# Optimization experiments

Hardware: AMD Instinct MI355X
Metric: run time of the kernel (lower is better)

The kernel has to match this reference:

```python
import jax, jax.numpy as jnp
import numpy as np

K = 3
STRIDE = 1
PAD = K // 2
GN_GROUPS = 32
EPS = 1e-5


def _conv(x, w, b, stride, pad):
    y = jax.lax.conv_general_dilated(
        x, w, window_strides=(stride, stride),
        padding=[(pad, pad), (pad, pad)],
        dimension_numbers=("NCHW", "OIHW", "NCHW"))
    return y + b[None, :, None, None]


def _bilinear_gather(img, ys, xs):
    # img: [B,C,H,W]; ys/xs: [B,P,Ho,Wo] float sampling coords (zero padding outside)
    B, C, H, W = img.shape
    y0 = jnp.floor(ys)
    x0 = jnp.floor(xs)
    y1, x1 = y0 + 1.0, x0 + 1.0
    wy1 = ys - y0  # weight toward y1
    wx1 = xs - x0
    wy0 = 1.0 - wy1
    wx0 = 1.0 - wx1
    img_flat = img.reshape(B, C, H * W)

    def corner(yc, xc, wgt):
        yi = yc.astype(jnp.int32)
        xi = xc.astype(jnp.int32)
        valid = (yi >= 0) & (yi < H) & (xi >= 0) & (xi < W)
        idx = jnp.clip(yi, 0, H - 1) * W + jnp.clip(xi, 0, W - 1)  # [B,P,Ho,Wo]
        Bp, P, Ho, Wo = idx.shape
        idx_f = jnp.broadcast_to(idx.reshape(B, 1, P * Ho * Wo), (B, C, P * Ho * Wo))
        vals = jnp.take_along_axis(img_flat, idx_f, axis=2).reshape(B, C, P, Ho, Wo)
        w_eff = jnp.where(valid, wgt, 0.0)[:, None]  # [B,1,P,Ho,Wo]
        return vals * w_eff

    out = (corner(y0, x0, wy0 * wx0) + corner(y0, x1, wy0 * wx1)
           + corner(y1, x0, wy1 * wx0) + corner(y1, x1, wy1 * wx1))
    return out  # [B,C,P,Ho,Wo]


def _deform_conv_gn_relu(x, w_off, b_off, w, b, gamma, beta):
    B, C_in, H, W = x.shape
    C_out = w.shape[0]
    P = K * K
    # offset-predicting conv: [B, 2*P, Ho, Wo], channel order (dy0,dx0,dy1,dx1,...)
    off = _conv(x, w_off, b_off, STRIDE, PAD)
    Ho, Wo = off.shape[2], off.shape[3]
    off = off.reshape(B, P, 2, Ho, Wo)
    dy, dx = off[:, :, 0], off[:, :, 1]  # [B,P,Ho,Wo]
    ky, kx = jnp.meshgrid(jnp.arange(K, dtype=x.dtype), jnp.arange(K, dtype=x.dtype), indexing="ij")
    ky, kx = ky.reshape(P), kx.reshape(P)
    base_y = (jnp.arange(Ho, dtype=x.dtype) * STRIDE - PAD)
    base_x = (jnp.arange(Wo, dtype=x.dtype) * STRIDE - PAD)
    ys = base_y[None, None, :, None] + ky[None, :, None, None] + dy
    xs = base_x[None, None, None, :] + kx[None, :, None, None] + dx
    cols = _bilinear_gather(x, ys, xs)  # [B,C_in,P,Ho,Wo]
    y = jnp.einsum("bcphw,ocp->bohw", cols, w.reshape(C_out, C_in, P)) + b[None, :, None, None]
    # GroupNorm(32, C_out)
    G = GN_GROUPS
    yg = y.reshape(B, G, (C_out // G) * Ho * Wo)
    mu = yg.mean(axis=2, keepdims=True)
    var = yg.var(axis=2, keepdims=True)
    yn = ((yg - mu) * jax.lax.rsqrt(var + EPS)).reshape(B, C_out, Ho, Wo)
    yn = yn * gamma[None, :, None, None] + beta[None, :, None, None]
    return jax.nn.relu(yn)


def setup_inputs() -> dict:
    key = jax.random.key(0)
    ks = jax.random.split(key, 7)
    B, C_in, C_out, H, W = 4, 256, 256, 64, 64
    P = K * K
    fan = C_in * P
    x = jax.random.normal(ks[0], (B, C_in, H, W), dtype=jnp.float32)
    w_off = jax.random.normal(ks[1], (2 * P, C_in, K, K), dtype=jnp.float32) * 0.01
    b_off = jnp.zeros((2 * P,), dtype=jnp.float32)
    w = jax.random.normal(ks[2], (C_out, C_in, K, K), dtype=jnp.float32) / np.sqrt(fan)
    b = jax.random.normal(ks[3], (C_out,), dtype=jnp.float32) * 0.01
    gamma = jnp.ones((C_out,), dtype=jnp.float32)
    beta = jnp.zeros((C_out,), dtype=jnp.float32)
    return {"x": x, "w_off": w_off, "b_off": b_off, "w": w, "b": b, "gamma": gamma, "beta": beta}


def reference(x, w_off, b_off, w, b, gamma, beta):
    return _deform_conv_gn_relu(x, w_off, b_off, w, b, gamma, beta)
```

## Files before the change

### kernel.cpp

```cpp
#include <hip/hip_runtime.h>
#include <hip/hip_bf16.h>

using bf16 = __hip_bfloat16;
typedef __attribute__((ext_vector_type(4))) float f32x4;
typedef __attribute__((ext_vector_type(2))) float f32x2;
typedef __attribute__((ext_vector_type(8))) __bf16 bf16x8;
typedef __attribute__((ext_vector_type(4))) __bf16 bf16x4;

#define CIN 256
#define COUT 256
#define HW 4096
#define NB 4
#define NTOT 16384
#define KDIM 2304

__global__ __launch_bounds__(256) void k_pre(const float* __restrict__ x,
                                             const float* __restrict__ w,
                                             const float* __restrict__ wof,
                                             bf16* __restrict__ xt,
                                             bf16* __restrict__ A,
                                             float* __restrict__ wt) {
  int bid = blockIdx.x;
  int tid = threadIdx.x;
  if (bid < 2048) {
    __shared__ float t[64][33];
    int ct = bid & 3;
    int hwt = (bid >> 2) & 127;
    int b = bid >> 9;
    int c0 = ct * 64, hw0 = hwt * 32;
    const float* xb = x + (size_t)b * CIN * HW;
    int cc = tid >> 5, ww = tid & 31;
#pragma unroll
    for (int pass = 0; pass < 8; ++pass)
      t[cc + pass * 8][ww] = xb[(size_t)(c0 + cc + pass * 8) * HW + hw0 + ww];
    __syncthreads();
    int hwl = tid >> 3, ce = (tid & 7) * 8;
    bf16x8 v;
#pragma unroll
    for (int e = 0; e < 8; ++e) v[e] = (__bf16)t[ce + e][hwl];
    *(bf16x8*)(xt + ((size_t)b * HW + hw0 + hwl) * CIN + c0 + ce) = v;
  } else if (bid < 4352) {
    int i = (bid - 2048) * 256 + tid;
    int o = i / KDIM, r = i % KDIM;
    int p = r >> 8, c = r & 255;
    A[i] = __float2bfloat16(w[((size_t)o * 256 + c) * 9 + p]);
  } else {
    int i = (bid - 4352) * 256 + tid;
    if (i < 18 * CIN * 9) {
      int oc = i % 18;
      int cp = i / 18;
      int c = cp / 9, p = cp % 9;
      wt[i] = wof[((size_t)oc * CIN + c) * 9 + p];
    }
  }
}

__global__ __launch_bounds__(256) void k_convoff2(const float* __restrict__ x,
                                                  const float* __restrict__ wt,
                                                  float* __restrict__ part) {
  __shared__ float lds[8][6][68];
  int bid = blockIdx.x;
  int chunk = bid & 7;
  int rt = (bid >> 3) & 15;
  int b = bid >> 7;
  int tid = threadIdx.x;
  int wq = tid & 63, r = tid >> 6;
  int h0 = rt * 4;
  int c0 = chunk * 32;

  if (tid < 96) {
    int cl = tid / 12, rem = tid % 12;
    lds[cl][rem >> 1][(rem & 1) ? 66 : 1] = 0.f;
  }

  float acc[18];
#pragma unroll
  for (int o = 0; o < 18; ++o) acc[o] = 0.f;

  int ch = tid >> 5, l32 = tid & 31;
  const float* xb = x + (size_t)b * CIN * HW;

  for (int cs = 0; cs < 32; cs += 8) {
    __syncthreads();
    const float* xp = xb + (size_t)(c0 + cs + ch) * HW;
#pragma unroll
    for (int r6 = 0; r6 < 6; ++r6) {
      int hh = h0 - 1 + r6;
      f32x2 v = {0.f, 0.f};
      if ((unsigned)hh < 64u) v = *(const f32x2*)(xp + hh * 64 + l32 * 2);
      *(f32x2*)&lds[ch][r6][2 + l32 * 2] = v;
    }
    __syncthreads();
#pragma unroll
    for (int cl = 0; cl < 8; ++cl) {
      int c = c0 + cs + cl;
      const float* wc = wt + (size_t)c * 9 * 18;
      float xv[9];
#pragma unroll
      for (int ky = 0; ky < 3; ++ky)
#pragma unroll
        for (int kx = 0; kx < 3; ++kx)
          xv[ky * 3 + kx] = lds[cl][r + ky][1 + wq + kx];
#pragma unroll
      for (int p = 0; p < 9; ++p)
#pragma unroll
        for (int o = 0; o < 18; ++o)
          acc[o] = fmaf(xv[p], wc[p * 18 + o], acc[o]);
    }
  }

  float* pp = part + (size_t)chunk * (NB * 18 * HW) + (size_t)b * 18 * HW +
              (h0 + r) * 64 + wq;
#pragma unroll
  for (int o = 0; o < 18; ++o) pp[(size_t)o * HW] = acc[o];
}

__global__ __launch_bounds__(256) void k_offreduce(const float* __restrict__ part,
                                                   const float* __restrict__ boff,
                                                   float* __restrict__ off) {
  int i = blockIdx.x * 256 + threadIdx.x;
  int e0 = i * 4;
  int oc = (e0 >> 12) % 18;
  float bo = boff[oc];
  f32x4 s = {bo, bo, bo, bo};
#pragma unroll
  for (int c = 0; c < 8; ++c) s += *(const f32x4*)(part + (size_t)c * (NB * 18 * HW) + e0);
  *(f32x4*)(off + e0) = s;
}

__global__ __launch_bounds__(256) void k_gather(const bf16* __restrict__ xt,
                                                const float* __restrict__ off,
                                                bf16* __restrict__ colsT) {
  int tid = threadIdx.x;
  int wv = tid >> 6, l = tid & 63;
  int n = blockIdx.x * 4 + wv;
  int hw = n & 4095;
  int b = n >> 12;
  int h = hw >> 6, wq = hw & 63;
  const bf16* xtb = xt + (size_t)b * HW * CIN + l * 4;
  const float* offb = off + (size_t)b * 18 * HW + hw;
  bf16* outp = colsT + (size_t)n * KDIM + l * 4;
#pragma unroll
  for (int p = 0; p < 9; ++p) {
    float dy = offb[(size_t)(2 * p) * HW];
    float dx = offb[(size_t)(2 * p + 1) * HW];
    float ysf = (float)(h - 1 + p / 3) + dy;
    float xsf = (float)(wq - 1 + p % 3) + dx;
    float y0f = floorf(ysf), x0f = floorf(xsf);
    float wy1 = ysf - y0f, wx1 = xsf - x0f;
    float wy0 = 1.f - wy1, wx0 = 1.f - wx1;
    int y0 = (int)y0f, x0 = (int)x0f;
    int y1 = y0 + 1, x1 = x0 + 1;
    float w00 = wy0 * wx0, w01 = wy0 * wx1, w10 = wy1 * wx0, w11 = wy1 * wx1;
    bool vy0 = (unsigned)y0 < 64u, vy1 = (unsigned)y1 < 64u;
    bool vx0 = (unsigned)x0 < 64u, vx1 = (unsigned)x1 < 64u;
    w00 = (vy0 && vx0) ? w00 : 0.f;
    w01 = (vy0 && vx1) ? w01 : 0.f;
    w10 = (vy1 && vx0) ? w10 : 0.f;
    w11 = (vy1 && vx1) ? w11 : 0.f;
    int y0c = min(max(y0, 0), 63), y1c = min(max(y1, 0), 63);
    int x0c = min(max(x0, 0), 63), x1c = min(max(x1, 0), 63);
    bf16x4 c00 = *(const bf16x4*)(xtb + (size_t)(y0c * 64 + x0c) * CIN);
    bf16x4 c01 = *(const bf16x4*)(xtb + (size_t)(y0c * 64 + x1c) * CIN);
    bf16x4 c10 = *(const bf16x4*)(xtb + (size_t)(y1c * 64 + x0c) * CIN);
    bf16x4 c11 = *(const bf16x4*)(xtb + (size_t)(y1c * 64 + x1c) * CIN);
    bf16x4 o;
#pragma unroll
    for (int k = 0; k < 4; ++k) {
      float v = w00 * (float)c00[k] + w01 * (float)c01[k] +
                w10 * (float)c10[k] + w11 * (float)c11[k];
      o[k] = (__bf16)v;
    }
    *(bf16x4*)(outp + p * 256) = o;
  }
}

__global__ __launch_bounds__(512) void k_gemm(const bf16* __restrict__ A,
                                              const bf16* __restrict__ Bt,
                                              const float* __restrict__ bias,
                                              bf16* __restrict__ Y0,
                                              bf16* __restrict__ Y1) {
  __shared__ bf16 As[2][256 * 64];
  __shared__ bf16 Bs[2][64 * 64];
  int bid = blockIdx.x;
  int swz = (bid & 7) * 64 + (bid >> 3);
  int n0 = (swz >> 1) * 64;
  int khalf = swz & 1;
  int tid = threadIdx.x;
  int lane = tid & 63;
  int wave = tid >> 6;
  int wr = (wave >> 1) * 64;
  int wc = (wave & 1) * 32;
  f32x4 acc[4][2];
#pragma unroll
  for (int i = 0; i < 4; ++i)
#pragma unroll
    for (int j = 0; j < 2; ++j) acc[i][j] = (f32x4){0.f, 0.f, 0.f, 0.f};

  int srow = tid >> 3;
  int skdst = (tid & 7) * 8;
  int sksrc = ((tid & 7) ^ ((tid >> 3) & 7)) * 8;
  int kbase = khalf * 18;
  auto stage = [&](int buf, int kt) {
    int k0 = (kbase + kt) * 64;
#pragma unroll
    for (int ps = 0; ps < 4; ++ps) {
      int r = srow + ps * 64;
      __builtin_amdgcn_global_load_lds(
          (const __attribute__((address_space(1))) void*)(A + (size_t)r * KDIM + k0 + sksrc),
          (__attribute__((address_space(3))) void*)(&As[buf][r * 64 + skdst]), 16, 0, 0);
    }
    __builtin_amdgcn_global_load_lds(
        (const __attribute__((address_space(1))) void*)(Bt + (size_t)(n0 + srow) * KDIM + k0 + sksrc),
        (__attribute__((address_space(3))) void*)(&Bs[buf][srow * 64 + skdst]), 16, 0, 0);
  };

  stage(0, 0);
  int rl = lane & 15;
  int kb = (lane >> 4) * 8;
  int xorv = (rl & 7) * 8;
  for (int kt = 0; kt < 18; ++kt) {
    __syncthreads();
    if (kt + 1 < 18) stage((kt + 1) & 1, kt + 1);
    const bf16* as = As[kt & 1];
    const bf16* bs = Bs[kt & 1];
#pragma unroll
    for (int kh = 0; kh < 2; ++kh) {
      int kc = (kh * 32 + kb) ^ xorv;
      bf16x8 af[4], bfr[2];
#pragma unroll
      for (int i = 0; i < 4; ++i)
        af[i] = *(const bf16x8*)(as + (wr + i * 16 + rl) * 64 + kc);
#pragma unroll
      for (int j = 0; j < 2; ++j)
        bfr[j] = *(const bf16x8*)(bs + (wc + j * 16 + rl) * 64 + kc);
#pragma unroll
      for (int i = 0; i < 4; ++i)
#pragma unroll
        for (int j = 0; j < 2; ++j)
          acc[i][j] = __builtin_amdgcn_mfma_f32_16x16x32_bf16(af[i], bfr[j], acc[i][j], 0, 0, 0);
    }
  }

  int cl = lane & 15, rg = (lane >> 4) * 4;
  bf16* Yp = khalf ? Y1 : Y0;
#pragma unroll
  for (int i = 0; i < 4; ++i) {
    int ob = wr + i * 16 + rg;
#pragma unroll
    for (int j = 0; j < 2; ++j) {
      int nn = n0 + wc + j * 16 + cl;
#pragma unroll
      for (int r = 0; r < 4; ++r) {
        float yv = acc[i][j][r] + (khalf ? 0.f : bias[ob + r]);
        Yp[(size_t)(ob + r) * NTOT + nn] = __float2bfloat16(yv);
      }
    }
  }
}

__global__ __launch_bounds__(1024) void k_gnapply(const bf16* __restrict__ Y0,
                                                  const bf16* __restrict__ Y1,
                                                  const float* __restrict__ gamma,
                                                  const float* __restrict__ beta,
                                                  float* __restrict__ out) {
  int bid = blockIdx.x;
  int b = bid >> 5, g = bid & 31;
  int tid = threadIdx.x;
  int ch = tid >> 7;
  int pos = (tid & 127) * 32;
  int o = g * 8 + ch;
  size_t off = (size_t)o * NTOT + b * HW + pos;
  float y[32];
#pragma unroll
  for (int q = 0; q < 4; ++q) {
    bf16x8 v0 = *(const bf16x8*)(Y0 + off + q * 8);
    bf16x8 v1 = *(const bf16x8*)(Y1 + off + q * 8);
#pragma unroll
    for (int k = 0; k < 8; ++k) y[q * 8 + k] = (float)v0[k] + (float)v1[k];
  }
  float s = 0.f, s2 = 0.f;
#pragma unroll
  for (int k = 0; k < 32; ++k) {
    s += y[k];
    s2 = fmaf(y[k], y[k], s2);
  }
  int lane = tid & 63, wv = tid >> 6;
#pragma unroll
  for (int mk = 1; mk <= 32; mk <<= 1) {
    s += __shfl_xor(s, mk);
    s2 += __shfl_xor(s2, mk);
  }
  __shared__ float red[32];
  __shared__ float stats[2];
  if (lane == 0) { red[wv] = s; red[wv + 16] = s2; }
  __syncthreads();
  if (tid == 0) {
    float S = 0.f, S2 = 0.f;
#pragma unroll
    for (int k = 0; k < 16; ++k) {
      S += red[k];
      S2 += red[k + 16];
    }
    float mu = S * (1.f / 32768.f);
    float var = S2 * (1.f / 32768.f) - mu * mu;
    stats[0] = mu;
    stats[1] = rsqrtf(var + 1e-5f);
  }
  __syncthreads();
  float mu = stats[0], rs = stats[1];
  float sc = rs * gamma[o];
  float sh = beta[o] - mu * sc;
  float* op = out + ((size_t)b * COUT + o) * HW + pos;
#pragma unroll
  for (int q = 0; q < 8; ++q) {
    f32x4 r;
#pragma unroll
    for (int k = 0; k < 4; ++k) r[k] = fmaxf(y[q * 4 + k] * sc + sh, 0.f);
    *(f32x4*)(op + q * 4) = r;
  }
}

extern "C" void kernel_launch(void* const* d_in, const int* in_sizes, int n_in,
                              void* d_out, int out_size, void* d_ws, size_t ws_size,
                              hipStream_t stream) {
  const float* x = (const float*)d_in[0];
  const float* w_off = (const float*)d_in[1];
  const float* b_off = (const float*)d_in[2];
  const float* w = (const float*)d_in[3];
  const float* bias = (const float*)d_in[4];
  const float* gamma = (const float*)d_in[5];
  const float* beta = (const float*)d_in[6];
  float* out = (float*)d_out;
  char* ws = (char*)d_ws;

  bf16* xt = (bf16*)(ws);
  float* offb = (float*)(ws + 8388608);
  bf16* Abf = (bf16*)(ws + 8388608 + 1179648);
  bf16* colsT = (bf16*)(ws + 8388608 + 2 * 1179648);
  bf16* Y0 = (bf16*)(ws + 8388608 + 2 * 1179648 + 75497472);
  bf16* Y1 = Y0 + (size_t)COUT * NTOT;

  float* wt = (float*)colsT;
  float* part = (float*)((char*)colsT + 262144);

  k_pre<<<4514, 256, 0, stream>>>(x, w, w_off, xt, Abf, wt);
  k_convoff2<<<512, 256, 0, stream>>>(x, wt, part);
  k_offreduce<<<288, 256, 0, stream>>>(part, b_off, offb);
  k_gather<<<4096, 256, 0, stream>>>(xt, offb, colsT);
  k_gemm<<<512, 512, 0, stream>>>(Abf, colsT, bias, Y0, Y1);
  k_gnapply<<<128, 1024, 0, stream>>>(Y0, Y1, gamma, beta, out);
}
```

Before: 117.6 us.

## Fuse offset conv into preprocessing kernel with LDS-staged offset weights

The separate offset-conv kernel is folded into the preprocessing kernel as extra blocks, so the x transpose, weight conversion and offset conv now run in a single launch. Each offset-conv block loads its 32-channel slice of the offset weights straight from the original layout into shared memory, which removes the global transposed-weight buffer and its write/read round trip. The cost is a larger shared allocation (about 33 KB) for every block of the fused kernel, including the transpose and conversion blocks that need much less, which can cut occupancy.

```diff
diff --git a/kernel.cpp b/kernel.cpp
--- a/kernel.cpp
+++ b/kernel.cpp
@@ -19,11 +19,12 @@
                                              const float* __restrict__ wof,
                                              bf16* __restrict__ xt,
                                              bf16* __restrict__ A,
-                                             float* __restrict__ wt) {
+                                             float* __restrict__ part) {
+  __shared__ float smem[8448];
   int bid = blockIdx.x;
   int tid = threadIdx.x;
   if (bid < 2048) {
-    __shared__ float t[64][33];
+    float (*t)[33] = (float(*)[33])smem;
     int ct = bid & 3;
     int hwt = (bid >> 2) & 127;
     int b = bid >> 9;
@@ -45,74 +46,66 @@
     int p = r >> 8, c = r & 255;
     A[i] = __float2bfloat16(w[((size_t)o * 256 + c) * 9 + p]);
   } else {
-    int i = (bid - 4352) * 256 + tid;
-    if (i < 18 * CIN * 9) {
-      int oc = i % 18;
-      int cp = i / 18;
-      int c = cp / 9, p = cp % 9;
-      wt[i] = wof[((size_t)oc * CIN + c) * 9 + p];
-    }
-  }
-}
-
-__global__ __launch_bounds__(256) void k_convoff2(const float* __restrict__ x,
-                                                  const float* __restrict__ wt,
-                                                  float* __restrict__ part) {
-  __shared__ float lds[8][6][68];
-  int bid = blockIdx.x;
-  int chunk = bid & 7;
-  int rt = (bid >> 3) & 15;
-  int b = bid >> 7;
-  int tid = threadIdx.x;
-  int wq = tid & 63, r = tid >> 6;
-  int h0 = rt * 4;
-  int c0 = chunk * 32;
-
-  if (tid < 96) {
-    int cl = tid / 12, rem = tid % 12;
-    lds[cl][rem >> 1][(rem & 1) ? 66 : 1] = 0.f;
-  }
-
-  float acc[18];
-#pragma unroll
-  for (int o = 0; o < 18; ++o) acc[o] = 0.f;
-
-  int ch = tid >> 5, l32 = tid & 31;
-  const float* xb = x + (size_t)b * CIN * HW;
-
-  for (int cs = 0; cs < 32; cs += 8) {
-    __syncthreads();
-    const float* xp = xb + (size_t)(c0 + cs + ch) * HW;
-#pragma unroll
-    for (int r6 = 0; r6 < 6; ++r6) {
-      int hh = h0 - 1 + r6;
-      f32x2 v = {0.f, 0.f};
-      if ((unsigned)hh < 64u) v = *(const f32x2*)(xp + hh * 64 + l32 * 2);
-      *(f32x2*)&lds[ch][r6][2 + l32 * 2] = v;
-    }
-    __syncthreads();
-#pragma unroll
-    for (int cl = 0; cl < 8; ++cl) {
-      int c = c0 + cs + cl;
-      const float* wc = wt + (size_t)c * 9 * 18;
-      float xv[9];
-#pragma unroll
-      for (int ky = 0; ky < 3; ++ky)
-#pragma unroll
-        for (int kx = 0; kx < 3; ++kx)
-          xv[ky * 3 + kx] = lds[cl][r + ky][1 + wq + kx];
-#pragma unroll
-      for (int p = 0; p < 9; ++p)
-#pragma unroll
-        for (int o = 0; o < 18; ++o)
-          acc[o] = fmaf(xv[p], wc[p * 18 + o], acc[o]);
-    }
-  }
-
-  float* pp = part + (size_t)chunk * (NB * 18 * HW) + (size_t)b * 18 * HW +
-              (h0 + r) * 64 + wq;
-#pragma unroll
-  for (int o = 0; o < 18; ++o) pp[(size_t)o * HW] = acc[o];
+    int cbid = bid - 4352;
+    int chunk = cbid & 7;
+    int rt = (cbid >> 3) & 15;
+    int b = cbid >> 7;
+    int wq = tid & 63, r = tid >> 6;
+    int h0 = rt * 4;
+    int c0 = chunk * 32;
+    float (*lds)[6][68] = (float(*)[6][68])smem;
+    float* wlds = smem + 3264;
+
+    for (int e = tid; e < 5184; e += 256) {
+      int cl = e / 162, rem = e % 162;
+      int p = rem / 18, oc = rem % 18;
+      wlds[e] = wof[((size_t)oc * CIN + c0 + cl) * 9 + p];
+    }
+    if (tid < 96) {
+      int cl = tid / 12, rem = tid % 12;
+      lds[cl][rem >> 1][(rem & 1) ? 66 : 1] = 0.f;
+    }
+
+    float acc[18];
+#pragma unroll
+    for (int o = 0; o < 18; ++o) acc[o] = 0.f;
+
+    int ch = tid >> 5, l32 = tid & 31;
+    const float* xb = x + (size_t)b * CIN * HW;
+
+    for (int cs = 0; cs < 32; cs += 8) {
+      __syncthreads();
+      const float* xp = xb + (size_t)(c0 + cs + ch) * HW;
+#pragma unroll
+      for (int r6 = 0; r6 < 6; ++r6) {
+        int hh = h0 - 1 + r6;
+        f32x2 v = {0.f, 0.f};
+        if ((unsigned)hh < 64u) v = *(const f32x2*)(xp + hh * 64 + l32 * 2);
+        *(f32x2*)&lds[ch][r6][2 + l32 * 2] = v;
+      }
+      __syncthreads();
+#pragma unroll
+      for (int cl = 0; cl < 8; ++cl) {
+        const float* wc = wlds + (cs + cl) * 162;
+        float xv[9];
+#pragma unroll
+        for (int ky = 0; ky < 3; ++ky)
+#pragma unroll
+          for (int kx = 0; kx < 3; ++kx)
+            xv[ky * 3 + kx] = lds[cl][r + ky][1 + wq + kx];
+#pragma unroll
+        for (int p = 0; p < 9; ++p)
+#pragma unroll
+          for (int o = 0; o < 18; ++o)
+            acc[o] = fmaf(xv[p], wc[p * 18 + o], acc[o]);
+      }
+    }
+
+    float* pp = part + (size_t)chunk * (NB * 18 * HW) + (size_t)b * 18 * HW +
+                (h0 + r) * 64 + wq;
+#pragma unroll
+    for (int o = 0; o < 18; ++o) pp[(size_t)o * HW] = acc[o];
+  }
 }
 
 __global__ __launch_bounds__(256) void k_offreduce(const float* __restrict__ part,
@@ -341,11 +334,9 @@
   bf16* Y0 = (bf16*)(ws + 8388608 + 2 * 1179648 + 75497472);
   bf16* Y1 = Y0 + (size_t)COUT * NTOT;
 
-  float* wt = (float*)colsT;
-  float* part = (float*)((char*)colsT + 262144);
-
-  k_pre<<<4514, 256, 0, stream>>>(x, w, w_off, xt, Abf, wt);
-  k_convoff2<<<512, 256, 0, stream>>>(x, wt, part);
+  float* part = (float*)colsT;
+
+  k_pre<<<4864, 256, 0, stream>>>(x, w, w_off, xt, Abf, part);
   k_offreduce<<<288, 256, 0, stream>>>(part, b_off, offb);
   k_gather<<<4096, 256, 0, stream>>>(xt, offb, colsT);
   k_gemm<<<512, 512, 0, stream>>>(Abf, colsT, bias, Y0, Y1);
```

New measurement: 129.0 us. 1.1x slower.
